# Performance work log

Hardware: AMD Instinct MI355X
Metric: run time of the kernel (lower is better)

## Reference

```python
import jax, jax.numpy as jnp
import numpy as np

B, NK, NQ, DK, DQ, H, DV = 16, 256, 256, 256, 256, 128, 256
MASK_VAL = -1000000.0

def setup_inputs() -> dict:
    key = jax.random.key(0)
    ks = jax.random.split(key, 7)
    return {
        "key": jax.random.normal(ks[0], (B, NK, DK), dtype=jnp.float32),
        "query": jax.random.normal(ks[1], (B, NQ, DQ), dtype=jnp.float32),
        "value": jax.random.normal(ks[2], (B, NQ, DV), dtype=jnp.float32),
        "valid_lens": jax.random.randint(ks[3], (B,), 1, NQ + 1, dtype=jnp.int32),
        "Wk": jax.random.normal(ks[4], (DK, H), dtype=jnp.float32) / np.sqrt(DK),
        "Wq": jax.random.normal(ks[5], (DQ, H), dtype=jnp.float32) / np.sqrt(DQ),
        "wv": jax.random.normal(ks[6], (H,), dtype=jnp.float32) / np.sqrt(H),
    }

def reference(key, query, value, valid_lens, Wk, Wq, wv):
    k = key @ Wk                      # (B, NK, H)
    q = query @ Wq                    # (B, NQ, H)
    # note: original unsqueezes key at dim 2, query at dim 1 -> (B, NK, NQ, H)
    feature = jnp.tanh(k[:, :, None, :] + q[:, None, :, :])
    scores = jnp.einsum('bkqh,h->bkq', feature, wv)   # (B, NK, NQ)
    # mask along last (query) axis per batch, as repeat_interleave does
    pos = jnp.arange(scores.shape[-1])[None, None, :]
    masked = jnp.where(pos < valid_lens[:, None, None], scores, MASK_VAL)
    attn = jax.nn.softmax(masked, axis=-1)            # (B, NK, NQ)
    return jnp.einsum('bkq,bqd->bkd', attn, value)    # (B, NK, DV)
```

## Files before the change

kernel.cpp:

```cpp
#include <hip/hip_runtime.h>

#define B_   16
#define NK_  256
#define NQ_  256
#define DK_  256
#define H_   128
#define DV_  256

#define C2X 2.8853900817779268f
#define L2E 1.4426950408889634f
#define MASKV -1.0e5f

typedef float f4 __attribute__((ext_vector_type(4)));

__device__ __forceinline__ float exp2_fast(float x) { return __builtin_amdgcn_exp2f(x); }
__device__ __forceinline__ float rcp_fast(float x)  { return __builtin_amdgcn_rcpf(x); }

__global__ __launch_bounds__(256) void proj_kernel(
    const float* __restrict__ key, const float* __restrict__ query,
    const float* __restrict__ Wk,  const float* __restrict__ Wq,
    float* __restrict__ kfE, float* __restrict__ qE4)
{
    __shared__ alignas(16) float A_s[32 * 256];
    __shared__ alignas(16) float W_s[64 * 128];

    const int blk = blockIdx.x;
    const int tid = threadIdx.x;
    const bool isQ = blk >= 128;
    const int rb = (blk & 127) * 32;

    const float* __restrict__ A = isQ ? query : key;
    const float* __restrict__ W = isQ ? Wq : Wk;

    {
        const f4* src = (const f4*)(A + (size_t)rb * DK_);
        f4* dst = (f4*)A_s;
#pragma unroll
        for (int j = 0; j < 8; ++j) dst[tid + 256 * j] = src[tid + 256 * j];
    }

    const int rg = (tid >> 5) * 4;
    const int c4 = (tid & 31) * 4;

    f4 acc[4];
#pragma unroll
    for (int r = 0; r < 4; ++r) acc[r] = (f4){0.f, 0.f, 0.f, 0.f};

    for (int kc = 0; kc < DK_; kc += 64) {
        __syncthreads();
        {
            const f4* wsrc = (const f4*)(W + (size_t)kc * H_);
            f4* wdst = (f4*)W_s;
#pragma unroll
            for (int j = 0; j < 8; ++j) wdst[tid + 256 * j] = wsrc[tid + 256 * j];
        }
        __syncthreads();
#pragma unroll 2
        for (int k = 0; k < 64; k += 4) {
            f4 w0 = *(const f4*)(W_s + (k + 0) * H_ + c4);
            f4 w1 = *(const f4*)(W_s + (k + 1) * H_ + c4);
            f4 w2 = *(const f4*)(W_s + (k + 2) * H_ + c4);
            f4 w3 = *(const f4*)(W_s + (k + 3) * H_ + c4);
#pragma unroll
            for (int r = 0; r < 4; ++r) {
                f4 a = *(const f4*)(A_s + (rg + r) * 256 + kc + k);
                acc[r] += a[0] * w0;
                acc[r] += a[1] * w1;
                acc[r] += a[2] * w2;
                acc[r] += a[3] * w3;
            }
        }
    }

    if (!isQ) {
        float* dst = kfE + (size_t)(rb + rg) * H_ + c4;
#pragma unroll
        for (int r = 0; r < 4; ++r) {
            f4 o;
#pragma unroll
            for (int cc = 0; cc < 4; ++cc) o[cc] = exp2_fast(C2X * acc[r][cc]);
            *(f4*)(dst + (size_t)r * H_) = o;
        }
    } else {
        const int b  = rb >> 8;
        const int q0 = (rb & 255) + rg;
        f4* dst = (f4*)qE4 + ((size_t)(b * 32 + (c4 >> 2))) * NQ_ + q0;
#pragma unroll
        for (int r = 0; r < 4; ++r) {
            f4 o;
#pragma unroll
            for (int cc = 0; cc < 4; ++cc) o[cc] = exp2_fast(C2X * acc[r][cc]);
            dst[r] = o;
        }
    }
}

__global__ __launch_bounds__(256) void attn_kernel(
    const float* __restrict__ kfE, const float* __restrict__ qE4,
    const float* __restrict__ value, const int* __restrict__ vlens,
    const float* __restrict__ wv, float* __restrict__ out)
{
    __shared__ alignas(16) float at4_s[256 * 4];
    __shared__ alignas(16) float red_s[16 * 256];

    const int x    = blockIdx.x;
    const int qu   = x >> 8;
    const int xi   = x & 255;
    const int b    = (xi + (qu << 2)) & 15;
    const int kt   = (xi >> 4) + (qu << 4);
    const int k0   = kt << 2;
    const int tid  = threadIdx.x;
    const int lane = tid & 63;
    const int wu   = __builtin_amdgcn_readfirstlane(tid >> 6);
    const int valid  = vlens[b];
    const int nchunk = (valid + 63) >> 6;

    float sumwv;
    {
        f4 sw = {0.f, 0.f, 0.f, 0.f};
#pragma unroll
        for (int i = 0; i < 32; ++i) sw += ((const f4*)wv)[i];
        sumwv = (sw[0] + sw[1]) + (sw[2] + sw[3]);
    }

    float accA[4], accB[4];
#pragma unroll
    for (int j = 0; j < 4; ++j) { accA[j] = 0.f; accB[j] = 0.f; }

    {
        const float* ekp = kfE + ((size_t)(b * NK_ + k0 + wu)) * H_;
        const f4*    eq0 = (const f4*)qE4 + (size_t)b * (32 * NQ_) + lane;

        auto run = [&](int NC) {
#pragma unroll 4
            for (int h4 = 0; h4 < 32; ++h4) {
                const f4 ek = *(const f4*)(ekp + (h4 << 2));
                const f4 w4 = *(const f4*)(wv  + (h4 << 2));
#pragma unroll
                for (int j = 0; j < 4; ++j) {
                    if (j >= NC) break;
                    const f4 eq = eq0[(size_t)h4 * NQ_ + (j << 6)];
                    accA[j] = fmaf(w4[0], rcp_fast(fmaf(ek[0], eq[0], 1.f)), accA[j]);
                    accB[j] = fmaf(w4[1], rcp_fast(fmaf(ek[1], eq[1], 1.f)), accB[j]);
                    accA[j] = fmaf(w4[2], rcp_fast(fmaf(ek[2], eq[2], 1.f)), accA[j]);
                    accB[j] = fmaf(w4[3], rcp_fast(fmaf(ek[3], eq[3], 1.f)), accB[j]);
                }
            }
        };
        switch (nchunk) {
            case 1: run(1); break;
            case 2: run(2); break;
            case 3: run(3); break;
            default: run(4); break;
        }
    }

    {
        float s[4];
#pragma unroll
        for (int j = 0; j < 4; ++j) {
            const int q = (j << 6) + lane;
            s[j] = (j < nchunk && q < valid)
                 ? (sumwv - 2.f * (accA[j] + accB[j])) : MASKV;
        }
        float m = fmaxf(fmaxf(s[0], s[1]), fmaxf(s[2], s[3]));
#pragma unroll
        for (int off = 32; off >= 1; off >>= 1)
            m = fmaxf(m, __shfl_xor(m, off, 64));
        float ssum = 0.f;
#pragma unroll
        for (int j = 0; j < 4; ++j) {
            s[j] = exp2_fast(L2E * (s[j] - m));
            ssum += s[j];
        }
#pragma unroll
        for (int off = 32; off >= 1; off >>= 1)
            ssum += __shfl_xor(ssum, off, 64);
        const float inv = rcp_fast(ssum);
#pragma unroll
        for (int j = 0; j < 4; ++j)
            at4_s[(((j << 6) + lane) << 2) + wu] = s[j] * inv;
    }
    __syncthreads();

    {
        const int rq = tid >> 6;
        const int d4 = lane << 2;
        const float* vb = value + (size_t)b * (NQ_ * DV_) + d4;
        f4 o0 = {0.f,0.f,0.f,0.f}, o1 = o0, o2 = o0, o3 = o0;
#pragma unroll 4
        for (int q = rq; q < valid; q += 4) {
            f4 v  = *(const f4*)(vb + (size_t)q * DV_);
            f4 a4 = *(const f4*)(at4_s + (q << 2));
            o0 += a4[0] * v;
            o1 += a4[1] * v;
            o2 += a4[2] * v;
            o3 += a4[3] * v;
        }
        float* rs = red_s + (rq << 10) + d4;
        *(f4*)(rs + 0)    = o0;
        *(f4*)(rs + 256)  = o1;
        *(f4*)(rs + 512)  = o2;
        *(f4*)(rs + 768)  = o3;
    }
    __syncthreads();

    {
        const int k  = tid >> 6;
        const int d4 = lane << 2;
        const float* rs = red_s + (k << 8) + d4;
        f4 o = *(const f4*)(rs) + *(const f4*)(rs + 1024)
             + *(const f4*)(rs + 2048) + *(const f4*)(rs + 3072);
        *(f4*)(out + ((size_t)(b * NK_ + k0 + k)) * DV_ + d4) = o;
    }
}

extern "C" void kernel_launch(void* const* d_in, const int* in_sizes, int n_in,
                              void* d_out, int out_size, void* d_ws, size_t ws_size,
                              hipStream_t stream)
{
    const float* key   = (const float*)d_in[0];
    const float* query = (const float*)d_in[1];
    const float* value = (const float*)d_in[2];
    const int*   vlens = (const int*)  d_in[3];
    const float* Wk    = (const float*)d_in[4];
    const float* Wq    = (const float*)d_in[5];
    const float* wv    = (const float*)d_in[6];
    float* outp = (float*)d_out;

    float* kfE = (float*)d_ws;
    float* qE4 = kfE + (size_t)B_ * NK_ * H_;

    hipLaunchKernelGGL(proj_kernel, dim3(256), dim3(256), 0, stream,
                       key, query, Wk, Wq, kfE, qE4);
    hipLaunchKernelGGL(attn_kernel, dim3(1024), dim3(256), 0, stream,
                       kfE, qE4, value, vlens, wv, outp);
}
```

Before: 103.5 us.

## Rebalance score work across waves and double projection grid size

The projection kernel now gives each block 16 rows instead of 32, which doubles the grid to 512 blocks for better CU occupancy. In the attention kernel, each wave used to compute scores for one key row over all valid query chunks. Now each wave handles a pair of key rows over alternating query chunks, so valid-length imbalance is spread across waves and each qE load is reused for two keys. Scores go through a new shared-memory buffer and an extra barrier before the per-row softmax, adding LDS traffic and sync in exchange for better load balance.

```diff
diff --git a/kernel.cpp b/kernel.cpp
--- a/kernel.cpp
+++ b/kernel.cpp
@@ -21,13 +21,13 @@
     const float* __restrict__ Wk,  const float* __restrict__ Wq,
     float* __restrict__ kfE, float* __restrict__ qE4)
 {
-    __shared__ alignas(16) float A_s[32 * 256];
+    __shared__ alignas(16) float A_s[16 * 256];
     __shared__ alignas(16) float W_s[64 * 128];
 
     const int blk = blockIdx.x;
     const int tid = threadIdx.x;
-    const bool isQ = blk >= 128;
-    const int rb = (blk & 127) * 32;
+    const bool isQ = blk >= 256;
+    const int rb = (blk & 255) * 16;
 
     const float* __restrict__ A = isQ ? query : key;
     const float* __restrict__ W = isQ ? Wq : Wk;
@@ -36,15 +36,13 @@
         const f4* src = (const f4*)(A + (size_t)rb * DK_);
         f4* dst = (f4*)A_s;
 #pragma unroll
-        for (int j = 0; j < 8; ++j) dst[tid + 256 * j] = src[tid + 256 * j];
-    }
-
-    const int rg = (tid >> 5) * 4;
-    const int c4 = (tid & 31) * 4;
-
-    f4 acc[4];
-#pragma unroll
-    for (int r = 0; r < 4; ++r) acc[r] = (f4){0.f, 0.f, 0.f, 0.f};
+        for (int j = 0; j < 4; ++j) dst[tid + 256 * j] = src[tid + 256 * j];
+    }
+
+    const int rg2 = (tid >> 5) << 1;
+    const int c4  = (tid & 31) << 2;
+
+    f4 acc0 = {0.f, 0.f, 0.f, 0.f}, acc1 = acc0;
 
     for (int kc = 0; kc < DK_; kc += 64) {
         __syncthreads();
@@ -61,37 +59,32 @@
             f4 w1 = *(const f4*)(W_s + (k + 1) * H_ + c4);
             f4 w2 = *(const f4*)(W_s + (k + 2) * H_ + c4);
             f4 w3 = *(const f4*)(W_s + (k + 3) * H_ + c4);
-#pragma unroll
-            for (int r = 0; r < 4; ++r) {
-                f4 a = *(const f4*)(A_s + (rg + r) * 256 + kc + k);
-                acc[r] += a[0] * w0;
-                acc[r] += a[1] * w1;
-                acc[r] += a[2] * w2;
-                acc[r] += a[3] * w3;
-            }
-        }
+            f4 a0 = *(const f4*)(A_s + (rg2 + 0) * 256 + kc + k);
+            f4 a1 = *(const f4*)(A_s + (rg2 + 1) * 256 + kc + k);
+            acc0 += a0[0] * w0; acc1 += a1[0] * w0;
+            acc0 += a0[1] * w1; acc1 += a1[1] * w1;
+            acc0 += a0[2] * w2; acc1 += a1[2] * w2;
+            acc0 += a0[3] * w3; acc1 += a1[3] * w3;
+        }
+    }
+
+    f4 e0, e1;
+#pragma unroll
+    for (int cc = 0; cc < 4; ++cc) {
+        e0[cc] = exp2_fast(C2X * acc0[cc]);
+        e1[cc] = exp2_fast(C2X * acc1[cc]);
     }
 
     if (!isQ) {
-        float* dst = kfE + (size_t)(rb + rg) * H_ + c4;
-#pragma unroll
-        for (int r = 0; r < 4; ++r) {
-            f4 o;
-#pragma unroll
-            for (int cc = 0; cc < 4; ++cc) o[cc] = exp2_fast(C2X * acc[r][cc]);
-            *(f4*)(dst + (size_t)r * H_) = o;
-        }
+        float* dst = kfE + (size_t)(rb + rg2) * H_ + c4;
+        *(f4*)(dst)      = e0;
+        *(f4*)(dst + H_) = e1;
     } else {
         const int b  = rb >> 8;
-        const int q0 = (rb & 255) + rg;
+        const int q0 = (rb & 255) + rg2;
         f4* dst = (f4*)qE4 + ((size_t)(b * 32 + (c4 >> 2))) * NQ_ + q0;
-#pragma unroll
-        for (int r = 0; r < 4; ++r) {
-            f4 o;
-#pragma unroll
-            for (int cc = 0; cc < 4; ++cc) o[cc] = exp2_fast(C2X * acc[r][cc]);
-            dst[r] = o;
-        }
+        dst[0] = e0;
+        dst[1] = e1;
     }
 }
 
@@ -100,6 +93,7 @@
     const float* __restrict__ value, const int* __restrict__ vlens,
     const float* __restrict__ wv, float* __restrict__ out)
 {
+    __shared__ alignas(16) float sc_s[4 * 260];
     __shared__ alignas(16) float at4_s[256 * 4];
     __shared__ alignas(16) float red_s[16 * 256];
 
@@ -123,47 +117,78 @@
         sumwv = (sw[0] + sw[1]) + (sw[2] + sw[3]);
     }
 
-    float accA[4], accB[4];
-#pragma unroll
-    for (int j = 0; j < 4; ++j) { accA[j] = 0.f; accB[j] = 0.f; }
-
-    {
-        const float* ekp = kfE + ((size_t)(b * NK_ + k0 + wu)) * H_;
-        const f4*    eq0 = (const f4*)qE4 + (size_t)b * (32 * NQ_) + lane;
-
-        auto run = [&](int NC) {
+    {
+        const int p   = wu >> 1;
+        const int par = wu & 1;
+        const int l0  = p << 1;
+        const int nslot = (par < nchunk ? 1 : 0) + (par + 2 < nchunk ? 1 : 0);
+
+        if (nslot) {
+            const float* ekp = kfE + ((size_t)(b * NK_ + k0 + l0)) * H_;
+            const f4*    eqA = (const f4*)qE4 + (size_t)b * (32 * NQ_)
+                               + ((par << 6) + lane);
+            const f4*    eqB = eqA + 128;
+
+            float acc[2][2][2];
+#pragma unroll
+            for (int s = 0; s < 2; ++s)
+#pragma unroll
+                for (int r = 0; r < 2; ++r) { acc[s][r][0] = 0.f; acc[s][r][1] = 0.f; }
+
+            auto body = [&](int NS) {
 #pragma unroll 4
-            for (int h4 = 0; h4 < 32; ++h4) {
-                const f4 ek = *(const f4*)(ekp + (h4 << 2));
-                const f4 w4 = *(const f4*)(wv  + (h4 << 2));
-#pragma unroll
-                for (int j = 0; j < 4; ++j) {
-                    if (j >= NC) break;
-                    const f4 eq = eq0[(size_t)h4 * NQ_ + (j << 6)];
-                    accA[j] = fmaf(w4[0], rcp_fast(fmaf(ek[0], eq[0], 1.f)), accA[j]);
-                    accB[j] = fmaf(w4[1], rcp_fast(fmaf(ek[1], eq[1], 1.f)), accB[j]);
-                    accA[j] = fmaf(w4[2], rcp_fast(fmaf(ek[2], eq[2], 1.f)), accA[j]);
-                    accB[j] = fmaf(w4[3], rcp_fast(fmaf(ek[3], eq[3], 1.f)), accB[j]);
+                for (int h4 = 0; h4 < 32; ++h4) {
+                    const f4 ekA = *(const f4*)(ekp + (h4 << 2));
+                    const f4 ekB = *(const f4*)(ekp + H_ + (h4 << 2));
+                    const f4 w4  = *(const f4*)(wv + (h4 << 2));
+                    {
+                        const f4 e = eqA[(size_t)h4 * NQ_];
+                        acc[0][0][0] = fmaf(w4[0], rcp_fast(fmaf(ekA[0], e[0], 1.f)), acc[0][0][0]);
+                        acc[0][0][1] = fmaf(w4[1], rcp_fast(fmaf(ekA[1], e[1], 1.f)), acc[0][0][1]);
+                        acc[0][0][0] = fmaf(w4[2], rcp_fast(fmaf(ekA[2], e[2], 1.f)), acc[0][0][0]);
+                        acc[0][0][1] = fmaf(w4[3], rcp_fast(fmaf(ekA[3], e[3], 1.f)), acc[0][0][1]);
+                        acc[0][1][0] = fmaf(w4[0], rcp_fast(fmaf(ekB[0], e[0], 1.f)), acc[0][1][0]);
+                        acc[0][1][1] = fmaf(w4[1], rcp_fast(fmaf(ekB[1], e[1], 1.f)), acc[0][1][1]);
+                        acc[0][1][0] = fmaf(w4[2], rcp_fast(fmaf(ekB[2], e[2], 1.f)), acc[0][1][0]);
+                        acc[0][1][1] = fmaf(w4[3], rcp_fast(fmaf(ekB[3], e[3], 1.f)), acc[0][1][1]);
+                    }
+                    if (NS == 2) {
+                        const f4 e = eqB[(size_t)h4 * NQ_];
+                        acc[1][0][0] = fmaf(w4[0], rcp_fast(fmaf(ekA[0], e[0], 1.f)), acc[1][0][0]);
+                        acc[1][0][1] = fmaf(w4[1], rcp_fast(fmaf(ekA[1], e[1], 1.f)), acc[1][0][1]);
+                        acc[1][0][0] = fmaf(w4[2], rcp_fast(fmaf(ekA[2], e[2], 1.f)), acc[1][0][0]);
+                        acc[1][0][1] = fmaf(w4[3], rcp_fast(fmaf(ekA[3], e[3], 1.f)), acc[1][0][1]);
+                        acc[1][1][0] = fmaf(w4[0], rcp_fast(fmaf(ekB[0], e[0], 1.f)), acc[1][1][0]);
+                        acc[1][1][1] = fmaf(w4[1], rcp_fast(fmaf(ekB[1], e[1], 1.f)), acc[1][1][1]);
+                        acc[1][1][0] = fmaf(w4[2], rcp_fast(fmaf(ekB[2], e[2], 1.f)), acc[1][1][0]);
+                        acc[1][1][1] = fmaf(w4[3], rcp_fast(fmaf(ekB[3], e[3], 1.f)), acc[1][1][1]);
+                    }
+                }
+            };
+            if (nslot == 1) body(1); else body(2);
+
+#pragma unroll
+            for (int s = 0; s < 2; ++s) {
+                if (s < nslot) {
+                    const int q = (((par + (s << 1))) << 6) + lane;
+                    sc_s[(l0 + 0) * 260 + q] = sumwv - 2.f * (acc[s][0][0] + acc[s][0][1]);
+                    sc_s[(l0 + 1) * 260 + q] = sumwv - 2.f * (acc[s][1][0] + acc[s][1][1]);
                 }
             }
-        };
-        switch (nchunk) {
-            case 1: run(1); break;
-            case 2: run(2); break;
-            case 3: run(3); break;
-            default: run(4); break;
-        }
-    }
-
-    {
+        }
+    }
+    __syncthreads();
+
+    {
+        const float* row = sc_s + wu * 260;
         float s[4];
+        float m = MASKV;
 #pragma unroll
         for (int j = 0; j < 4; ++j) {
             const int q = (j << 6) + lane;
-            s[j] = (j < nchunk && q < valid)
-                 ? (sumwv - 2.f * (accA[j] + accB[j])) : MASKV;
-        }
-        float m = fmaxf(fmaxf(s[0], s[1]), fmaxf(s[2], s[3]));
+            s[j] = (q < valid) ? row[q] : MASKV;
+            m = fmaxf(m, s[j]);
+        }
 #pragma unroll
         for (int off = 32; off >= 1; off >>= 1)
             m = fmaxf(m, __shfl_xor(m, off, 64));
@@ -231,7 +256,7 @@
     float* kfE = (float*)d_ws;
     float* qE4 = kfE + (size_t)B_ * NK_ * H_;
 
-    hipLaunchKernelGGL(proj_kernel, dim3(256), dim3(256), 0, stream,
+    hipLaunchKernelGGL(proj_kernel, dim3(512), dim3(256), 0, stream,
                        key, query, Wk, Wq, kfE, qE4);
     hipLaunchKernelGGL(attn_kernel, dim3(1024), dim3(256), 0, stream,
                        kfE, qE4, value, vlens, wv, outp);
```

Result: faster. 101.1 us (-2.2%).
